# Kernel optimization log

Measured on AMD Instinct MI355X. Metric: run time of the kernel, lower is better.

## Reference

```python
import jax, jax.numpy as jnp
import numpy as np

N = 50000      # num_nodes
E = 800000     # num_edges
H = 64         # hidden_dim
L = 4          # num_layers
NH = 4         # num_heads
HD = H // NH   # head_dim


def setup_inputs() -> dict:
    key = jax.random.key(0)
    ks = iter(jax.random.split(key, 64))
    def nrm(shape, s=0.1):
        return jax.random.normal(next(ks), shape, jnp.float32) * s
    inp = dict(
        x=jax.random.normal(next(ks), (N, 4), jnp.float32),
        edge_index=jax.random.randint(next(ks), (2, E), 0, N),
        edge_attr=jax.random.normal(next(ks), (E, 2), jnp.float32),
        in_w=nrm((4, H)), in_b=jnp.zeros((H,), jnp.float32),
        conv_rw1=nrm((L, H + 2, H)), conv_rb1=jnp.zeros((L, H), jnp.float32),
        conv_rw2=nrm((L, H, H)), conv_rb2=jnp.zeros((L, H), jnp.float32),
        conv_iw1=nrm((L, H + 2, H)), conv_ib1=jnp.zeros((L, H), jnp.float32),
        conv_iw2=nrm((L, H, H)), conv_ib2=jnp.zeros((L, H), jnp.float32),
        conv_sw=nrm((L, H, 4 * H)), conv_sb=jnp.zeros((L, 4 * H), jnp.float32),
        att_qw=nrm((L, 4, H)), att_qb=jnp.zeros((L, H), jnp.float32),
        att_kw=nrm((L, 4, H)), att_kb=jnp.zeros((L, H), jnp.float32),
        att_vw=nrm((L, 4, H)), att_vb=jnp.zeros((L, H), jnp.float32),
        att_ow=nrm((L, H, 4)), att_ob=jnp.zeros((L, 4), jnp.float32),
        ln_g=jnp.ones((L, 4), jnp.float32), ln_b=jnp.zeros((L, 4), jnp.float32),
        out_w1=nrm((H, H // 2)), out_b1=jnp.zeros((H // 2,), jnp.float32),
        out_w2=nrm((H // 2, 4)), out_b2=jnp.zeros((4,), jnp.float32),
        res_w=jnp.full((L,), 0.1, jnp.float32),
    )
    return inp


def reference(x, edge_index, edge_attr, in_w, in_b,
              conv_rw1, conv_rb1, conv_rw2, conv_rb2,
              conv_iw1, conv_ib1, conv_iw2, conv_ib2,
              conv_sw, conv_sb,
              att_qw, att_qb, att_kw, att_kb, att_vw, att_vb, att_ow, att_ob,
              ln_g, ln_b, out_w1, out_b1, out_w2, out_b2, res_w):
    n = x.shape[0]
    row, col = edge_index[0], edge_index[1]
    # add_self_loops with edge_attr fill 0 (used only inside the conv)
    loops = jnp.arange(n)
    row_sl = jnp.concatenate([row, loops])
    col_sl = jnp.concatenate([col, loops])
    ea_sl = jnp.concatenate([edge_attr, jnp.zeros((n, 2), edge_attr.dtype)], axis=0)
    deg = jax.ops.segment_sum(jnp.ones((row_sl.shape[0],), x.dtype), col_sl,
                              num_segments=n)[:, None]  # >=1 due to self loops

    h = x @ in_w + in_b  # [N, H]
    for i in range(L):
        residual = x
        # ---- ComplexGraphConv (mean aggregation, source_to_target) ----
        msg_in = jnp.concatenate([h[row_sl], ea_sl], axis=-1)  # [E+N, H+2]
        real = jax.nn.relu(msg_in @ conv_rw1[i] + conv_rb1[i]) @ conv_rw2[i] + conv_rb2[i]
        imag = jax.nn.relu(msg_in @ conv_iw1[i] + conv_ib1[i]) @ conv_iw2[i] + conv_ib2[i]
        mag = jnp.sqrt(real * real + imag * imag)
        phase = jnp.arctan2(imag, real + 1e-8)
        msg = jnp.concatenate([real, imag, mag, phase], axis=-1)  # [E+N, 4H]
        agg = jax.ops.segment_sum(msg, col_sl, num_segments=n) / deg
        h4 = agg + (h @ conv_sw[i] + conv_sb[i])  # [N, 4H]
        x4 = h4[:, :4]
        # ---- ComplexGraphAttention (global edge softmax per head) ----
        Q = (x4 @ att_qw[i] + att_qb[i]).reshape(n, NH, HD)
        K = (x4 @ att_kw[i] + att_kb[i]).reshape(n, NH, HD)
        V = (x4 @ att_vw[i] + att_vb[i]).reshape(n, NH, HD)
        scores = jnp.einsum('ehd,ehd->eh', Q[row], K[col]) / np.sqrt(HD).astype(x.dtype)
        w = jax.nn.softmax(scores, axis=0)  # softmax over ALL edges (dim=0)
        att = jax.ops.segment_sum(w[:, :, None] * V[row], col,
                                  num_segments=n).reshape(n, NH * HD)
        x4 = (att @ att_ow[i] + att_ob[i]) + x4  # out_proj + residual (dropout=eval)
        # ---- LayerNorm over last dim (4) ----
        mu = x4.mean(-1, keepdims=True)
        var = x4.var(-1, keepdims=True)
        x4 = (x4 - mu) / jnp.sqrt(var + 1e-5) * ln_g[i] + ln_b[i]
        x = x4 + residual * res_w[i]
        h = x @ in_w + in_b
    pred = jnp.tanh(jax.nn.relu(h @ out_w1 + out_b1) @ out_w2 + out_b2) * 0.3
    return pred
```

## Files before the change

### kernel.cpp

```cpp
#include <hip/hip_runtime.h>
#include <hip/hip_bf16.h>
#include <hip/hip_fp16.h>

#define N_NODES 50000
#define N_EDGES 800000
#define BUCKET 64
#define EDGE_TB 3125
#define NODE_NB 3125

__device__ __forceinline__ float rdlane(float v, int k) {
    return __uint_as_float(__builtin_amdgcn_readlane(__float_as_uint(v), k));
}
template <int CTRL>
__device__ __forceinline__ float dpp_addf(float v) {
    int x = __builtin_amdgcn_update_dpp(0, __float_as_int(v), CTRL, 0xF, 0xF, true);
    return v + __int_as_float(x);
}
#define DPP_QX1  0xB1
#define DPP_QX2  0x4E
#define DPP_HM   0x141
#define DPP_RM   0x140
#define DPP_ROR4 0x124
#define DPP_ROR8 0x128
__device__ __forceinline__ float dpp_sum16(float v) {
    v = dpp_addf<DPP_QX1>(v);
    v = dpp_addf<DPP_QX2>(v);
    v = dpp_addf<DPP_HM>(v);
    v = dpp_addf<DPP_RM>(v);
    return v;
}
__device__ __forceinline__ void bsum4(float& v0, float& v1, float& v2, float& v3) {
    #pragma unroll
    for (int m = 1; m < 64; m <<= 1) {
        v0 += __shfl_xor(v0, m);
        v1 += __shfl_xor(v1, m);
        v2 += __shfl_xor(v2, m);
        v3 += __shfl_xor(v3, m);
    }
}
__device__ __forceinline__ void cvt_t4(float2 raw, float tk[4]) {
    __half2 a = ((const __half2*)&raw)[0];
    __half2 b = ((const __half2*)&raw)[1];
    float2 fa = __half22float2(a), fb = __half22float2(b);
    tk[0] = fa.x; tk[1] = fa.y; tk[2] = fb.x; tk[3] = fb.y;
}

__global__ void k_setup(const float* __restrict__ x, const float* __restrict__ in_w,
                        const float* __restrict__ in_b, const float* __restrict__ rw1,
                        const float* __restrict__ rb1, float* __restrict__ hb,
                        float4* __restrict__ xcur, unsigned* __restrict__ cntC,
                        __half* __restrict__ t,
                        const int* __restrict__ row, const int* __restrict__ col,
                        const float* __restrict__ ea, uint2* __restrict__ colEA,
                        const float* __restrict__ qw, const float* __restrict__ qb,
                        const float* __restrict__ kw, const float* __restrict__ kb,
                        const float* __restrict__ vw, const float* __restrict__ vb,
                        const float* __restrict__ ow, float* __restrict__ cst,
                        float* __restrict__ cstV) {
    int tid = threadIdx.x;
    int bid = blockIdx.x;
    if (bid < 2 * EDGE_TB) {
        if ((bid & 1) == 0) {
            int e = (bid >> 1) * 256 + tid;
            if (e < N_EDGES) {
                int c = col[e];
                unsigned slot = atomicAdd(&cntC[c], 1u);
                float2 e2 = ((const float2*)ea)[e];
                __half2 h2 = __floats2half2_rn(e2.x, e2.y);
                unsigned long long rec =
                    ((unsigned long long)(unsigned)row[e] << 32) |
                    (unsigned long long)(*reinterpret_cast<unsigned*>(&h2));
                __builtin_nontemporal_store(
                    rec, (unsigned long long*)&colEA[(size_t)c * BUCKET + slot]);
            }
            return;
        }
        int wid = ((bid >> 1) * 256 + tid) >> 6;
        int lane = tid & 63;
        int n0 = wid * 4;
        if (n0 >= N_NODES) return;
        float iw0 = in_w[lane], iw1 = in_w[64 + lane], iw2 = in_w[128 + lane], iw3 = in_w[192 + lane];
        float ibl = in_b[lane];
        float hv[4];
        #pragma unroll
        for (int i = 0; i < 4; i++) {
            int n = n0 + i;
            hv[i] = 0.f;
            if (n < N_NODES) {
                float4 xv = ((const float4*)x)[n];
                hv[i] = ibl + xv.x * iw0 + xv.y * iw1 + xv.z * iw2 + xv.w * iw3;
                hb[n * 64 + lane] = hv[i];
                if (lane == 0) xcur[n] = xv;
            }
        }
        float acc[4];
        #pragma unroll
        for (int i = 0; i < 4; i++) acc[i] = rb1[lane];
        for (int k = 0; k < 64; k++) {
            float w = rw1[k * 64 + lane];
            #pragma unroll
            for (int i = 0; i < 4; i++) acc[i] += rdlane(hv[i], k) * w;
        }
        #pragma unroll
        for (int i = 0; i < 4; i++) {
            int n = n0 + i;
            if (n < N_NODES) t[n * 64 + lane] = __float2half(acc[i]);
        }
        return;
    }
    int pb = bid - 2 * EDGE_TB;
    int m = tid;
    if (m >= 64) return;
    int d = m & 15;
    if (pb < 4) {
        int L = pb;
        const float* qwl = qw + L * 256; const float* kwl = kw + L * 256;
        const float* qbl = qb + L * 64;  const float* kbl = kb + L * 64;
        float qa[4], ka[4];
        #pragma unroll
        for (int a = 0; a < 4; a++) { qa[a] = qwl[a * 64 + m]; ka[a] = kwl[a * 64 + m]; }
        float qbm = qbl[m], kbm = kbl[m];
        float vals[25];
        int idx = 0;
        #pragma unroll
        for (int a = 0; a < 4; a++)
            #pragma unroll
            for (int b = 0; b < 4; b++) vals[idx++] = qa[a] * ka[b];
        #pragma unroll
        for (int a = 0; a < 4; a++) vals[idx++] = qa[a] * kbm;
        #pragma unroll
        for (int b = 0; b < 4; b++) vals[idx++] = qbm * ka[b];
        vals[24] = qbm * kbm;
        #pragma unroll
        for (int i = 0; i < 25; i++) {
            float v = vals[i];
            v += __shfl_xor(v, 1); v += __shfl_xor(v, 2);
            v += __shfl_xor(v, 4); v += __shfl_xor(v, 8);
            vals[i] = v;
        }
        if (d == 0) {
            float* out = cst + L * 128 + (m >> 4) * 32;
            #pragma unroll
            for (int i = 0; i < 25; i++) out[i] = vals[i] * 0.25f;
        }
    } else {
        int L = pb - 4;
        int h = m >> 4;
        const float* vwl = vw + L * 256;
        const float* vbl = vb + L * 64;
        float4 owv = ((const float4*)(ow + L * 256))[m];
        float vals[20];
        #pragma unroll
        for (int a = 0; a < 4; a++) {
            float v = vwl[a * 64 + m];
            vals[a * 4 + 0] = v * owv.x; vals[a * 4 + 1] = v * owv.y;
            vals[a * 4 + 2] = v * owv.z; vals[a * 4 + 3] = v * owv.w;
        }
        float b = vbl[m];
        vals[16] = b * owv.x; vals[17] = b * owv.y; vals[18] = b * owv.z; vals[19] = b * owv.w;
        #pragma unroll
        for (int i = 0; i < 20; i++) {
            float v = vals[i];
            v += __shfl_xor(v, 1); v += __shfl_xor(v, 2);
            v += __shfl_xor(v, 4); v += __shfl_xor(v, 8);
            vals[i] = v;
        }
        if (d == 0) {
            float* out = cstV + L * 128 + h * 32;
            #pragma unroll
            for (int i = 0; i < 20; i++) out[i] = vals[i];
        }
    }
}

__global__ void k61(const float* __restrict__ att16, const float* __restrict__ sumexpP,
                    const float4* __restrict__ x4b, const float* __restrict__ ob,
                    const float* __restrict__ g, const float* __restrict__ bb,
                    const float* __restrict__ resw, const float* __restrict__ in_w,
                    const float* __restrict__ in_b, float4* __restrict__ xcur,
                    const float* __restrict__ rw1, const float* __restrict__ rb1,
                    __half* __restrict__ t, float* __restrict__ hb) {
    int tid = threadIdx.x;
    int wid = (blockIdx.x * blockDim.x + tid) >> 6;
    int lane = tid & 63;
    int n0 = wid * 4;
    if (n0 >= N_NODES) return;
    float iw0 = in_w[lane], iw1 = in_w[64 + lane], iw2 = in_w[128 + lane], iw3 = in_w[192 + lane];
    float ibl = in_b[lane];
    float4 zp = ((const float4*)sumexpP)[lane];
    bsum4(zp.x, zp.y, zp.z, zp.w);
    int hh = (lane & 15) >> 2;
    float z = (hh == 0) ? zp.x : (hh == 1) ? zp.y : (hh == 2) ? zp.z : zp.w;
    float ob0 = ob[0], ob1 = ob[1], ob2 = ob[2], ob3 = ob[3];
    float g0 = g[0], g1 = g[1], g2 = g[2], g3 = g[3];
    float bb0 = bb[0], bb1 = bb[1], bb2 = bb[2], bb3 = bb[3];
    float rw = resw[0];
    float hv[4];
    #pragma unroll
    for (int i = 0; i < 4; i++) {
        int n = n0 + i;
        float a = 0.f;
        if (n < N_NODES && lane < 16) a = att16[n * 16 + lane] / z;
        a = dpp_addf<DPP_ROR4>(a);
        a = dpp_addf<DPP_ROR8>(a);
        float y0 = rdlane(a, 0), y1 = rdlane(a, 1), y2 = rdlane(a, 2), y3 = rdlane(a, 3);
        hv[i] = 0.f;
        if (n < N_NODES) {
            float4 x4v = x4b[n];
            y0 += ob0 + x4v.x; y1 += ob1 + x4v.y;
            y2 += ob2 + x4v.z; y3 += ob3 + x4v.w;
            float mu = 0.25f * (y0 + y1 + y2 + y3);
            float d0 = y0 - mu, d1 = y1 - mu, d2 = y2 - mu, d3 = y3 - mu;
            float var = 0.25f * (d0 * d0 + d1 * d1 + d2 * d2 + d3 * d3);
            float rs = rsqrtf(var + 1e-5f);
            float4 xold = xcur[n];
            float nn0 = d0 * rs * g0 + bb0 + xold.x * rw;
            float nn1 = d1 * rs * g1 + bb1 + xold.y * rw;
            float nn2 = d2 * rs * g2 + bb2 + xold.z * rw;
            float nn3 = d3 * rs * g3 + bb3 + xold.w * rw;
            if (lane == 0) xcur[n] = make_float4(nn0, nn1, nn2, nn3);
            hv[i] = ibl + nn0 * iw0 + nn1 * iw1 + nn2 * iw2 + nn3 * iw3;
            hb[n * 64 + lane] = hv[i];
        }
    }
    float acc[4];
    #pragma unroll
    for (int i = 0; i < 4; i++) acc[i] = rb1[lane];
    for (int k = 0; k < 64; k++) {
        float w = rw1[k * 64 + lane];
        #pragma unroll
        for (int i = 0; i < 4; i++) acc[i] += rdlane(hv[i], k) * w;
    }
    #pragma unroll
    for (int i = 0; i < 4; i++) {
        int n = n0 + i;
        if (n < N_NODES) t[n * 64 + lane] = __float2half(acc[i]);
    }
}

__global__ void k23b(const unsigned* __restrict__ cntC, const uint2* __restrict__ colEA,
                     const __half* __restrict__ t, const float* __restrict__ hb,
                     const float* __restrict__ rw1, const float* __restrict__ rw2,
                     const float* __restrict__ sw, const float* __restrict__ rb2,
                     const float* __restrict__ sb,
                     float4* __restrict__ x4b, float* __restrict__ sumexpP) {
    __shared__ float s_rw2[64][4];
    __shared__ float s_sw[64][4];
    __shared__ float s_w1[128];
    int tid = threadIdx.x;
    { int r = tid >> 2, cc = tid & 3; s_rw2[r][cc] = rw2[r * 64 + cc]; s_sw[r][cc] = sw[r * 256 + cc]; }
    if (tid < 128) s_w1[tid] = rw1[64 * 64 + tid];
    if (blockIdx.x == 0) sumexpP[tid] = 0.f;
    __syncthreads();
    int lane = tid & 63;
    int sub = lane >> 4, l16 = lane & 15;
    int gid = (blockIdx.x * blockDim.x + tid) >> 6;
    int c = gid * 4 + sub;
    if (c >= N_NODES) return;
    float w1a[4], w1b[4], wr2[4][4];
    #pragma unroll
    for (int j = 0; j < 4; j++) {
        int ch = l16 * 4 + j;
        w1a[j] = s_w1[ch];
        w1b[j] = s_w1[64 + ch];
        #pragma unroll
        for (int o = 0; o < 4; o++) wr2[j][o] = s_rw2[ch][o];
    }
    float2 trS = *(const float2*)(t + (size_t)c * 64 + l16 * 4);
    float4 hv = ((const float4*)hb)[c * 16 + l16];
    float a0 = 0.f, a1 = 0.f, a2 = 0.f, a3 = 0.f;
    float b0 = 0.f, b1 = 0.f, b2 = 0.f, b3 = 0.f;
    {
        float tk[4];
        cvt_t4(trS, tk);
        #pragma unroll
        for (int j = 0; j < 4; j++) {
            int ch = l16 * 4 + j;
            float rr = fmaxf(tk[j], 0.f);
            a0 += rr * wr2[j][0]; a1 += rr * wr2[j][1];
            a2 += rr * wr2[j][2]; a3 += rr * wr2[j][3];
            float hk = (j == 0) ? hv.x : (j == 1) ? hv.y : (j == 2) ? hv.z : hv.w;
            b0 += hk * s_sw[ch][0]; b1 += hk * s_sw[ch][1];
            b2 += hk * s_sw[ch][2]; b3 += hk * s_sw[ch][3];
        }
    }
    int cnt = (int)cntC[c];
    const uint2* rowE = colEA + (size_t)c * BUCKET;
    const uint2 zr = make_uint2(0u, 0u);
    const float2 z2 = make_float2(0.f, 0.f);
    int p = 0;
    bool vld0 = p < cnt;
    uint2 erA = vld0 ? rowE[0] : zr;
    float2 trA = vld0 ? *(const float2*)(t + (size_t)erA.y * 64 + l16 * 4) : z2;
    int pn = 1;
    bool vld1 = pn < cnt;
    uint2 erB = vld1 ? rowE[1] : zr;
    while (vld0) {
        float2 trB = vld1 ? *(const float2*)(t + (size_t)erB.y * 64 + l16 * 4) : z2;
        int pnn = pn + 1;
        bool vld2 = pnn < cnt;
        uint2 erC = vld2 ? rowE[pnn] : zr;
        float tk[4];
        cvt_t4(trA, tk);
        __half2 eh = *reinterpret_cast<const __half2*>(&erA.x);
        float2 ef = __half22float2(eh);
        float ex = ef.x, ey = ef.y;
        #pragma unroll
        for (int j = 0; j < 4; j++) {
            float pre = tk[j] + ex * w1a[j] + ey * w1b[j];
            float rr = fmaxf(pre, 0.f);
            a0 += rr * wr2[j][0]; a1 += rr * wr2[j][1];
            a2 += rr * wr2[j][2]; a3 += rr * wr2[j][3];
        }
        erA = erB; trA = trB; erB = erC;
        vld0 = vld1; vld1 = vld2; pn = pnn;
    }
    a0 = dpp_sum16(a0); a1 = dpp_sum16(a1); a2 = dpp_sum16(a2); a3 = dpp_sum16(a3);
    b0 = dpp_sum16(b0); b1 = dpp_sum16(b1); b2 = dpp_sum16(b2); b3 = dpp_sum16(b3);
    if (l16 == 0) {
        float idg = 1.f / (float)(cnt + 1);
        x4b[c] = make_float4(a0 * idg + b0 + rb2[0] + sb[0],
                             a1 * idg + b1 + rb2[1] + sb[1],
                             a2 * idg + b2 + rb2[2] + sb[2],
                             a3 * idg + b3 + rb2[3] + sb[3]);
    }
}

__global__ void k5_att(const unsigned* __restrict__ cntC, const uint2* __restrict__ colEA,
                       const float4* __restrict__ x4b, const float* __restrict__ cst,
                       const float* __restrict__ cstV, float* __restrict__ att16,
                       float* __restrict__ sumexpP) {
    __shared__ float zs[8][4];
    int tid = threadIdx.x;
    int lane = tid & 63;
    int wv = tid >> 6;
    int hw = lane >> 5;
    int l32 = lane & 31;
    int sub = l32 >> 4;
    int d = l32 & 15, h = d >> 2, a = d & 3;
    int c = ((blockIdx.x * blockDim.x + tid) >> 6) * 2 + hw;
    float zval = 0.f;
    if (c < N_NODES) {
        const float* C = cst + h * 32;
        float4 xc = x4b[c];
        float g0 = xc.x * C[0]  + xc.y * C[1]  + xc.z * C[2]  + xc.w * C[3]  + C[16];
        float g1 = xc.x * C[4]  + xc.y * C[5]  + xc.z * C[6]  + xc.w * C[7]  + C[17];
        float g2 = xc.x * C[8]  + xc.y * C[9]  + xc.z * C[10] + xc.w * C[11] + C[18];
        float g3 = xc.x * C[12] + xc.y * C[13] + xc.z * C[14] + xc.w * C[15] + C[19];
        float base = C[20] * xc.x + C[21] * xc.y + C[22] * xc.z + C[23] * xc.w + C[24];
        int cnt = (int)cntC[c];
        const unsigned* rowY = (const unsigned*)(colEA + (size_t)c * BUCKET);
        const float4 z4 = make_float4(0.f, 0.f, 0.f, 0.f);
        float S = 0.f, z = 0.f;
        int p = sub;
        bool vld0 = p < cnt;
        float4 xr = z4;
        if (vld0) xr = x4b[rowY[2 * p + 1]];
        int pn = p + 2;
        bool vld1 = pn < cnt;
        unsigned rn = vld1 ? rowY[2 * pn + 1] : 0u;
        while (vld0) {
            float4 xrn = z4;
            if (vld1) xrn = x4b[rn];
            int pnn = pn + 2;
            bool vld2 = pnn < cnt;
            unsigned rnn = vld2 ? rowY[2 * pnn + 1] : 0u;
            float s = xr.x * g0 + xr.y * g1 + xr.z * g2 + xr.w * g3 + base;
            float ex = __expf(s);
            float xa = (a == 0) ? xr.x : (a == 1) ? xr.y : (a == 2) ? xr.z : xr.w;
            S += ex * xa;
            z += ex;
            xr = xrn; rn = rnn; vld0 = vld1; vld1 = vld2; pn = pnn;
        }
        S += __shfl_xor(S, 16);
        z += __shfl_xor(z, 16);
        const float* V = cstV + h * 32;
        float c0 = S * V[a * 4 + 0], c1 = S * V[a * 4 + 1];
        float c2 = S * V[a * 4 + 2], c3 = S * V[a * 4 + 3];
        c0 = dpp_addf<DPP_QX1>(c0); c1 = dpp_addf<DPP_QX1>(c1);
        c2 = dpp_addf<DPP_QX1>(c2); c3 = dpp_addf<DPP_QX1>(c3);
        c0 = dpp_addf<DPP_QX2>(c0); c1 = dpp_addf<DPP_QX2>(c1);
        c2 = dpp_addf<DPP_QX2>(c2); c3 = dpp_addf<DPP_QX2>(c3);
        float my = (a == 0) ? c0 : (a == 1) ? c1 : (a == 2) ? c2 : c3;
        if (sub == 0) att16[c * 16 + d] = my + z * V[16 + a];
        zval = z;
    }
    if (sub == 0 && a == 0) zs[wv * 2 + hw][h] = zval;
    __syncthreads();
    if (tid < 4) {
        float acc = 0.f;
        #pragma unroll
        for (int q = 0; q < 8; q++) acc += zs[q][tid];
        atomicAdd(&sumexpP[((blockIdx.x & 63) << 2) + tid], acc);
    }
}

__global__ void k6pred(const float* __restrict__ att16, const float* __restrict__ sumexpP,
                       const float4* __restrict__ x4b, const float* __restrict__ ob,
                       const float* __restrict__ g, const float* __restrict__ bb,
                       const float* __restrict__ resw, const float4* __restrict__ xcur,
                       const float* __restrict__ in_w, const float* __restrict__ in_b,
                       const float* __restrict__ w1, const float* __restrict__ b1,
                       const float* __restrict__ w2, const float* __restrict__ b2,
                       float* __restrict__ out) {
    int tid = threadIdx.x;
    int node = (blockIdx.x * blockDim.x + tid) >> 6;
    int lane = tid & 63;
    if (node >= N_NODES) return;
    float4 zp = ((const float4*)sumexpP)[lane];
    bsum4(zp.x, zp.y, zp.z, zp.w);
    int hh = (lane & 15) >> 2;
    float z = (hh == 0) ? zp.x : (hh == 1) ? zp.y : (hh == 2) ? zp.z : zp.w;
    float a = 0.f;
    if (lane < 16) a = att16[node * 16 + lane] / z;
    a = dpp_addf<DPP_ROR4>(a);
    a = dpp_addf<DPP_ROR8>(a);
    float y0 = rdlane(a, 0), y1 = rdlane(a, 1), y2 = rdlane(a, 2), y3 = rdlane(a, 3);
    float4 x4v = x4b[node];
    y0 += ob[0] + x4v.x; y1 += ob[1] + x4v.y;
    y2 += ob[2] + x4v.z; y3 += ob[3] + x4v.w;
    float mu = 0.25f * (y0 + y1 + y2 + y3);
    float d0 = y0 - mu, d1 = y1 - mu, d2 = y2 - mu, d3 = y3 - mu;
    float var = 0.25f * (d0 * d0 + d1 * d1 + d2 * d2 + d3 * d3);
    float rs = rsqrtf(var + 1e-5f);
    float4 xold = xcur[node];
    float rw = resw[0];
    float n0 = d0 * rs * g[0] + bb[0] + xold.x * rw;
    float n1 = d1 * rs * g[1] + bb[1] + xold.y * rw;
    float n2 = d2 * rs * g[2] + bb[2] + xold.z * rw;
    float n3 = d3 * rs * g[3] + bb[3] + xold.w * rw;
    float hv = in_b[lane] + n0 * in_w[lane] + n1 * in_w[64 + lane]
             + n2 * in_w[128 + lane] + n3 * in_w[192 + lane];
    int j2 = lane & 31;
    float m = b1[j2];
    for (int k = 0; k < 64; k++) m += rdlane(hv, k) * w1[k * 32 + j2];
    m = fmaxf(m, 0.f);
    float4 w2v = ((const float4*)w2)[j2];
    float v0 = m * w2v.x, v1 = m * w2v.y, v2 = m * w2v.z, v3 = m * w2v.w;
    bsum4(v0, v1, v2, v3);
    float o0 = tanhf(0.5f * v0 + b2[0]) * 0.3f;
    float o1 = tanhf(0.5f * v1 + b2[1]) * 0.3f;
    float o2 = tanhf(0.5f * v2 + b2[2]) * 0.3f;
    float o3 = tanhf(0.5f * v3 + b2[3]) * 0.3f;
    if (lane == 0) ((float4*)out)[node] = make_float4(o0, o1, o2, o3);
}

extern "C" void kernel_launch(void* const* d_in, const int* in_sizes, int n_in,
                              void* d_out, int out_size, void* d_ws, size_t ws_size,
                              hipStream_t stream) {
    const float* x        = (const float*)d_in[0];
    const int*   ei       = (const int*)d_in[1];
    const float* ea       = (const float*)d_in[2];
    const float* in_w     = (const float*)d_in[3];
    const float* in_b     = (const float*)d_in[4];
    const float* conv_rw1 = (const float*)d_in[5];
    const float* conv_rb1 = (const float*)d_in[6];
    const float* conv_rw2 = (const float*)d_in[7];
    const float* conv_rb2 = (const float*)d_in[8];
    const float* conv_sw  = (const float*)d_in[13];
    const float* conv_sb  = (const float*)d_in[14];
    const float* att_qw   = (const float*)d_in[15];
    const float* att_qb   = (const float*)d_in[16];
    const float* att_kw   = (const float*)d_in[17];
    const float* att_kb   = (const float*)d_in[18];
    const float* att_vw   = (const float*)d_in[19];
    const float* att_vb   = (const float*)d_in[20];
    const float* att_ow   = (const float*)d_in[21];
    const float* att_ob   = (const float*)d_in[22];
    const float* ln_g     = (const float*)d_in[23];
    const float* ln_b     = (const float*)d_in[24];
    const float* out_w1   = (const float*)d_in[25];
    const float* out_b1   = (const float*)d_in[26];
    const float* out_w2   = (const float*)d_in[27];
    const float* out_b2   = (const float*)d_in[28];
    const float* res_w    = (const float*)d_in[29];

    const int* row = ei;
    const int* col = ei + N_EDGES;

    char* ws = (char*)d_ws;
    size_t off = 0;
    auto alloc = [&](size_t bytes) -> void* {
        void* p = ws + off;
        off = (off + bytes + 255) & ~(size_t)255;
        return p;
    };
    unsigned* cntC     = (unsigned*)alloc(N_NODES * 4);
    uint2*    colEA    = (uint2*)alloc((size_t)N_NODES * BUCKET * 8);
    __half*   tbuf     = (__half*)alloc((size_t)N_NODES * 64 * 2);
    float*    hb       = (float*)alloc((size_t)N_NODES * 64 * 4);
    float*    att16    = (float*)alloc((size_t)N_NODES * 16 * 4);
    float4*   x4b      = (float4*)alloc((size_t)N_NODES * 16);
    float4*   xcur     = (float4*)alloc((size_t)N_NODES * 16);
    float*    cst      = (float*)alloc(4 * 128 * 4);
    float*    cstV     = (float*)alloc(4 * 128 * 4);
    float*    sumexpP  = (float*)alloc(64 * 4 * 4);

    dim3 b256(256);
    int nodeBlocks2 = (N_NODES + 7) / 8;
    int nodeBlocks4 = (N_NODES + 15) / 16;
    int dstBlocks   = (N_NODES + 15) / 16;

    hipMemsetAsync(cntC, 0, N_NODES * 4, stream);
    k_setup<<<2 * EDGE_TB + 8, b256, 0, stream>>>(
        x, in_w, in_b, conv_rw1, conv_rb1, hb, xcur, cntC, tbuf,
        row, col, ea, colEA,
        att_qw, att_qb, att_kw, att_kb, att_vw, att_vb, att_ow, cst, cstV);

    for (int i = 0; i < 4; i++) {
        const float* rw1 = conv_rw1 + i * 66 * 64;
        const float* rb1 = conv_rb1 + i * 64;
        const float* rw2 = conv_rw2 + i * 64 * 64;
        const float* rb2 = conv_rb2 + i * 64;
        const float* swl = conv_sw + i * 64 * 256;
        const float* sbl = conv_sb + i * 256;

        if (i > 0) {
            k61<<<nodeBlocks4, b256, 0, stream>>>(att16, sumexpP, x4b,
                                                  att_ob + (i - 1) * 4, ln_g + (i - 1) * 4,
                                                  ln_b + (i - 1) * 4, res_w + (i - 1),
                                                  in_w, in_b, xcur,
                                                  rw1, rb1, tbuf, hb);
        }
        k23b<<<dstBlocks, b256, 0, stream>>>(cntC, colEA, tbuf, hb,
                                             rw1, rw2, swl, rb2, sbl, x4b, sumexpP);
        k5_att<<<nodeBlocks2, b256, 0, stream>>>(cntC, colEA, x4b, cst + i * 128,
                                                 cstV + i * 128, att16, sumexpP);
    }
    k6pred<<<(N_NODES + 3) / 4, b256, 0, stream>>>(att16, sumexpP, x4b, att_ob + 12, ln_g + 12,
                                            ln_b + 12, res_w + 3, xcur, in_w, in_b,
                                            out_w1, out_b1, out_w2, out_b2, (float*)d_out);
}
```

Measured before the change: 497.2 us.

## Fold input projection into conv weights and gather 4-wide node state per edge

Since h = x @ in_w + in_b is an affine map of the 4-wide node state, the first conv layer's pre-activation and the skip projection are folded into small precomputed matrices (in_w·rw1, in_b·rw1+rb1, in_w·sw). The per-node 64-wide fp16 t buffer and fp32 h buffer are no longer materialized. The edge loop now gathers a 16-byte float4 of xcur per source node instead of a 64-channel fp16 slice, and recomputes the 64-channel preactivation with extra FMAs per edge. This trades DRAM/L2 gather traffic and the k61 matmul for more ALU work per edge, and it also removes fp16 rounding of t.

```diff
diff --git a/kernel.cpp b/kernel.cpp
--- a/kernel.cpp
+++ b/kernel.cpp
@@ -6,7 +6,7 @@
 #define N_EDGES 800000
 #define BUCKET 64
 #define EDGE_TB 3125
-#define NODE_NB 3125
+#define COPY_NB 196
 
 __device__ __forceinline__ float rdlane(float v, int k) {
     return __uint_as_float(__builtin_amdgcn_readlane(__float_as_uint(v), k));
@@ -38,77 +38,43 @@
         v3 += __shfl_xor(v3, m);
     }
 }
-__device__ __forceinline__ void cvt_t4(float2 raw, float tk[4]) {
-    __half2 a = ((const __half2*)&raw)[0];
-    __half2 b = ((const __half2*)&raw)[1];
-    float2 fa = __half22float2(a), fb = __half22float2(b);
-    tk[0] = fa.x; tk[1] = fa.y; tk[2] = fb.x; tk[3] = fb.y;
-}
-
-__global__ void k_setup(const float* __restrict__ x, const float* __restrict__ in_w,
-                        const float* __restrict__ in_b, const float* __restrict__ rw1,
-                        const float* __restrict__ rb1, float* __restrict__ hb,
-                        float4* __restrict__ xcur, unsigned* __restrict__ cntC,
-                        __half* __restrict__ t,
+
+__global__ void k_setup(const float* __restrict__ x, unsigned* __restrict__ cntC,
+                        float4* __restrict__ xcur,
                         const int* __restrict__ row, const int* __restrict__ col,
                         const float* __restrict__ ea, uint2* __restrict__ colEA,
                         const float* __restrict__ qw, const float* __restrict__ qb,
                         const float* __restrict__ kw, const float* __restrict__ kb,
                         const float* __restrict__ vw, const float* __restrict__ vb,
-                        const float* __restrict__ ow, float* __restrict__ cst,
-                        float* __restrict__ cstV) {
+                        const float* __restrict__ ow,
+                        const float* __restrict__ in_w, const float* __restrict__ in_b,
+                        const float* __restrict__ rw1all, const float* __restrict__ rb1all,
+                        const float* __restrict__ swall,
+                        float* __restrict__ cst, float* __restrict__ cstV,
+                        float* __restrict__ cstM) {
     int tid = threadIdx.x;
     int bid = blockIdx.x;
-    if (bid < 2 * EDGE_TB) {
-        if ((bid & 1) == 0) {
-            int e = (bid >> 1) * 256 + tid;
-            if (e < N_EDGES) {
-                int c = col[e];
-                unsigned slot = atomicAdd(&cntC[c], 1u);
-                float2 e2 = ((const float2*)ea)[e];
-                __half2 h2 = __floats2half2_rn(e2.x, e2.y);
-                unsigned long long rec =
-                    ((unsigned long long)(unsigned)row[e] << 32) |
-                    (unsigned long long)(*reinterpret_cast<unsigned*>(&h2));
-                __builtin_nontemporal_store(
-                    rec, (unsigned long long*)&colEA[(size_t)c * BUCKET + slot]);
-            }
-            return;
-        }
-        int wid = ((bid >> 1) * 256 + tid) >> 6;
-        int lane = tid & 63;
-        int n0 = wid * 4;
-        if (n0 >= N_NODES) return;
-        float iw0 = in_w[lane], iw1 = in_w[64 + lane], iw2 = in_w[128 + lane], iw3 = in_w[192 + lane];
-        float ibl = in_b[lane];
-        float hv[4];
-        #pragma unroll
-        for (int i = 0; i < 4; i++) {
-            int n = n0 + i;
-            hv[i] = 0.f;
-            if (n < N_NODES) {
-                float4 xv = ((const float4*)x)[n];
-                hv[i] = ibl + xv.x * iw0 + xv.y * iw1 + xv.z * iw2 + xv.w * iw3;
-                hb[n * 64 + lane] = hv[i];
-                if (lane == 0) xcur[n] = xv;
-            }
-        }
-        float acc[4];
-        #pragma unroll
-        for (int i = 0; i < 4; i++) acc[i] = rb1[lane];
-        for (int k = 0; k < 64; k++) {
-            float w = rw1[k * 64 + lane];
-            #pragma unroll
-            for (int i = 0; i < 4; i++) acc[i] += rdlane(hv[i], k) * w;
-        }
-        #pragma unroll
-        for (int i = 0; i < 4; i++) {
-            int n = n0 + i;
-            if (n < N_NODES) t[n * 64 + lane] = __float2half(acc[i]);
+    if (bid < EDGE_TB) {
+        int e = bid * 256 + tid;
+        if (e < N_EDGES) {
+            int c = col[e];
+            unsigned slot = atomicAdd(&cntC[c], 1u);
+            float2 e2 = ((const float2*)ea)[e];
+            __half2 h2 = __floats2half2_rn(e2.x, e2.y);
+            unsigned long long rec =
+                ((unsigned long long)(unsigned)row[e] << 32) |
+                (unsigned long long)(*reinterpret_cast<unsigned*>(&h2));
+            __builtin_nontemporal_store(
+                rec, (unsigned long long*)&colEA[(size_t)c * BUCKET + slot]);
         }
         return;
     }
-    int pb = bid - 2 * EDGE_TB;
+    if (bid < EDGE_TB + COPY_NB) {
+        int n = (bid - EDGE_TB) * 256 + tid;
+        if (n < N_NODES) xcur[n] = ((const float4*)x)[n];
+        return;
+    }
+    int pb = bid - (EDGE_TB + COPY_NB);
     int m = tid;
     if (m >= 64) return;
     int d = m & 15;
@@ -143,7 +109,7 @@
             #pragma unroll
             for (int i = 0; i < 25; i++) out[i] = vals[i] * 0.25f;
         }
-    } else {
+    } else if (pb < 8) {
         int L = pb - 4;
         int h = m >> 4;
         const float* vwl = vw + L * 256;
@@ -170,23 +136,47 @@
             #pragma unroll
             for (int i = 0; i < 20; i++) out[i] = vals[i];
         }
+    } else {
+        int L = pb - 8;
+        const float* rw1 = rw1all + L * 66 * 64;
+        const float* rb1 = rb1all + L * 64;
+        const float* sw  = swall + L * 64 * 256;
+        float* M = cstM + L * 384;
+        float bacc = rb1[m];
+        float w0 = 0.f, w1 = 0.f, w2 = 0.f, w3 = 0.f;
+        for (int k = 0; k < 64; k++) {
+            float r = rw1[k * 64 + m];
+            bacc += in_b[k] * r;
+            w0 += in_w[k] * r;
+            w1 += in_w[64 + k] * r;
+            w2 += in_w[128 + k] * r;
+            w3 += in_w[192 + k] * r;
+        }
+        M[m * 4 + 0] = w0; M[m * 4 + 1] = w1; M[m * 4 + 2] = w2; M[m * 4 + 3] = w3;
+        M[256 + m] = bacc;
+        if (m < 16) {
+            int a = m >> 2, o = m & 3;
+            float sacc = 0.f;
+            for (int k = 0; k < 64; k++) sacc += in_w[a * 64 + k] * sw[k * 256 + o];
+            M[320 + m] = sacc;
+        }
+        if (m < 4) {
+            float sacc = 0.f;
+            for (int k = 0; k < 64; k++) sacc += in_b[k] * sw[k * 256 + m];
+            M[336 + m] = sacc;
+        }
     }
 }
 
 __global__ void k61(const float* __restrict__ att16, const float* __restrict__ sumexpP,
                     const float4* __restrict__ x4b, const float* __restrict__ ob,
                     const float* __restrict__ g, const float* __restrict__ bb,
-                    const float* __restrict__ resw, const float* __restrict__ in_w,
-                    const float* __restrict__ in_b, float4* __restrict__ xcur,
-                    const float* __restrict__ rw1, const float* __restrict__ rb1,
-                    __half* __restrict__ t, float* __restrict__ hb) {
+                    const float* __restrict__ resw, float4* __restrict__ xcur) {
     int tid = threadIdx.x;
     int wid = (blockIdx.x * blockDim.x + tid) >> 6;
     int lane = tid & 63;
     int n0 = wid * 4;
     if (n0 >= N_NODES) return;
-    float iw0 = in_w[lane], iw1 = in_w[64 + lane], iw2 = in_w[128 + lane], iw3 = in_w[192 + lane];
-    float ibl = in_b[lane];
     float4 zp = ((const float4*)sumexpP)[lane];
     bsum4(zp.x, zp.y, zp.z, zp.w);
     int hh = (lane & 15) >> 2;
@@ -195,7 +185,6 @@
     float g0 = g[0], g1 = g[1], g2 = g[2], g3 = g[3];
     float bb0 = bb[0], bb1 = bb[1], bb2 = bb[2], bb3 = bb[3];
     float rw = resw[0];
-    float hv[4];
     #pragma unroll
     for (int i = 0; i < 4; i++) {
         int n = n0 + i;
@@ -204,7 +193,6 @@
         a = dpp_addf<DPP_ROR4>(a);
         a = dpp_addf<DPP_ROR8>(a);
         float y0 = rdlane(a, 0), y1 = rdlane(a, 1), y2 = rdlane(a, 2), y3 = rdlane(a, 3);
-        hv[i] = 0.f;
         if (n < N_NODES) {
             float4 x4v = x4b[n];
             y0 += ob0 + x4v.x; y1 += ob1 + x4v.y;
@@ -219,37 +207,27 @@
             float nn2 = d2 * rs * g2 + bb2 + xold.z * rw;
             float nn3 = d3 * rs * g3 + bb3 + xold.w * rw;
             if (lane == 0) xcur[n] = make_float4(nn0, nn1, nn2, nn3);
-            hv[i] = ibl + nn0 * iw0 + nn1 * iw1 + nn2 * iw2 + nn3 * iw3;
-            hb[n * 64 + lane] = hv[i];
-        }
-    }
-    float acc[4];
-    #pragma unroll
-    for (int i = 0; i < 4; i++) acc[i] = rb1[lane];
-    for (int k = 0; k < 64; k++) {
-        float w = rw1[k * 64 + lane];
-        #pragma unroll
-        for (int i = 0; i < 4; i++) acc[i] += rdlane(hv[i], k) * w;
-    }
-    #pragma unroll
-    for (int i = 0; i < 4; i++) {
-        int n = n0 + i;
-        if (n < N_NODES) t[n * 64 + lane] = __float2half(acc[i]);
+        }
     }
 }
 
 __global__ void k23b(const unsigned* __restrict__ cntC, const uint2* __restrict__ colEA,
-                     const __half* __restrict__ t, const float* __restrict__ hb,
-                     const float* __restrict__ rw1, const float* __restrict__ rw2,
-                     const float* __restrict__ sw, const float* __restrict__ rb2,
-                     const float* __restrict__ sb,
+                     const float4* __restrict__ xcur, const float* __restrict__ rw1,
+                     const float* __restrict__ rw2, const float* __restrict__ cstM,
+                     const float* __restrict__ rb2, const float* __restrict__ sb,
                      float4* __restrict__ x4b, float* __restrict__ sumexpP) {
     __shared__ float s_rw2[64][4];
-    __shared__ float s_sw[64][4];
+    __shared__ float s_weff[64][4];
     __shared__ float s_w1[128];
+    __shared__ float s_beff[64];
+    __shared__ float s_sw16[16];
+    __shared__ float s_sbe[4];
     int tid = threadIdx.x;
-    { int r = tid >> 2, cc = tid & 3; s_rw2[r][cc] = rw2[r * 64 + cc]; s_sw[r][cc] = sw[r * 256 + cc]; }
+    { int r = tid >> 2, cc = tid & 3; s_rw2[r][cc] = rw2[r * 64 + cc]; s_weff[r][cc] = cstM[tid]; }
     if (tid < 128) s_w1[tid] = rw1[64 * 64 + tid];
+    if (tid < 64) s_beff[tid] = cstM[256 + tid];
+    if (tid < 16) s_sw16[tid] = cstM[320 + tid];
+    if (tid < 4)  s_sbe[tid]  = cstM[336 + tid];
     if (blockIdx.x == 0) sumexpP[tid] = 0.f;
     __syncthreads();
     int lane = tid & 63;
@@ -257,68 +235,65 @@
     int gid = (blockIdx.x * blockDim.x + tid) >> 6;
     int c = gid * 4 + sub;
     if (c >= N_NODES) return;
-    float w1a[4], w1b[4], wr2[4][4];
+    float wf[4][4], bfr[4], w1a[4], w1b[4], wr2r[4][4];
     #pragma unroll
     for (int j = 0; j < 4; j++) {
         int ch = l16 * 4 + j;
+        #pragma unroll
+        for (int a = 0; a < 4; a++) wf[j][a] = s_weff[ch][a];
+        bfr[j] = s_beff[ch];
         w1a[j] = s_w1[ch];
         w1b[j] = s_w1[64 + ch];
         #pragma unroll
-        for (int o = 0; o < 4; o++) wr2[j][o] = s_rw2[ch][o];
-    }
-    float2 trS = *(const float2*)(t + (size_t)c * 64 + l16 * 4);
-    float4 hv = ((const float4*)hb)[c * 16 + l16];
+        for (int o = 0; o < 4; o++) wr2r[j][o] = s_rw2[ch][o];
+    }
+    float4 xc = xcur[c];
     float a0 = 0.f, a1 = 0.f, a2 = 0.f, a3 = 0.f;
-    float b0 = 0.f, b1 = 0.f, b2 = 0.f, b3 = 0.f;
-    {
-        float tk[4];
-        cvt_t4(trS, tk);
-        #pragma unroll
-        for (int j = 0; j < 4; j++) {
-            int ch = l16 * 4 + j;
-            float rr = fmaxf(tk[j], 0.f);
-            a0 += rr * wr2[j][0]; a1 += rr * wr2[j][1];
-            a2 += rr * wr2[j][2]; a3 += rr * wr2[j][3];
-            float hk = (j == 0) ? hv.x : (j == 1) ? hv.y : (j == 2) ? hv.z : hv.w;
-            b0 += hk * s_sw[ch][0]; b1 += hk * s_sw[ch][1];
-            b2 += hk * s_sw[ch][2]; b3 += hk * s_sw[ch][3];
-        }
+    #pragma unroll
+    for (int j = 0; j < 4; j++) {
+        float tk = bfr[j] + xc.x * wf[j][0] + xc.y * wf[j][1]
+                 + xc.z * wf[j][2] + xc.w * wf[j][3];
+        float rr = fmaxf(tk, 0.f);
+        a0 += rr * wr2r[j][0]; a1 += rr * wr2r[j][1];
+        a2 += rr * wr2r[j][2]; a3 += rr * wr2r[j][3];
     }
     int cnt = (int)cntC[c];
     const uint2* rowE = colEA + (size_t)c * BUCKET;
     const uint2 zr = make_uint2(0u, 0u);
-    const float2 z2 = make_float2(0.f, 0.f);
+    const float4 z4 = make_float4(0.f, 0.f, 0.f, 0.f);
     int p = 0;
     bool vld0 = p < cnt;
     uint2 erA = vld0 ? rowE[0] : zr;
-    float2 trA = vld0 ? *(const float2*)(t + (size_t)erA.y * 64 + l16 * 4) : z2;
+    float4 xrA = vld0 ? xcur[erA.y] : z4;
     int pn = 1;
     bool vld1 = pn < cnt;
     uint2 erB = vld1 ? rowE[1] : zr;
     while (vld0) {
-        float2 trB = vld1 ? *(const float2*)(t + (size_t)erB.y * 64 + l16 * 4) : z2;
+        float4 xrB = vld1 ? xcur[erB.y] : z4;
         int pnn = pn + 1;
         bool vld2 = pnn < cnt;
         uint2 erC = vld2 ? rowE[pnn] : zr;
-        float tk[4];
-        cvt_t4(trA, tk);
         __half2 eh = *reinterpret_cast<const __half2*>(&erA.x);
         float2 ef = __half22float2(eh);
-        float ex = ef.x, ey = ef.y;
         #pragma unroll
         for (int j = 0; j < 4; j++) {
-            float pre = tk[j] + ex * w1a[j] + ey * w1b[j];
+            float tk = bfr[j] + xrA.x * wf[j][0] + xrA.y * wf[j][1]
+                     + xrA.z * wf[j][2] + xrA.w * wf[j][3];
+            float pre = tk + ef.x * w1a[j] + ef.y * w1b[j];
             float rr = fmaxf(pre, 0.f);
-            a0 += rr * wr2[j][0]; a1 += rr * wr2[j][1];
-            a2 += rr * wr2[j][2]; a3 += rr * wr2[j][3];
-        }
-        erA = erB; trA = trB; erB = erC;
+            a0 += rr * wr2r[j][0]; a1 += rr * wr2r[j][1];
+            a2 += rr * wr2r[j][2]; a3 += rr * wr2r[j][3];
+        }
+        erA = erB; xrA = xrB; erB = erC;
         vld0 = vld1; vld1 = vld2; pn = pnn;
     }
     a0 = dpp_sum16(a0); a1 = dpp_sum16(a1); a2 = dpp_sum16(a2); a3 = dpp_sum16(a3);
-    b0 = dpp_sum16(b0); b1 = dpp_sum16(b1); b2 = dpp_sum16(b2); b3 = dpp_sum16(b3);
     if (l16 == 0) {
         float idg = 1.f / (float)(cnt + 1);
+        float b0 = xc.x * s_sw16[0] + xc.y * s_sw16[4] + xc.z * s_sw16[8]  + xc.w * s_sw16[12] + s_sbe[0];
+        float b1 = xc.x * s_sw16[1] + xc.y * s_sw16[5] + xc.z * s_sw16[9]  + xc.w * s_sw16[13] + s_sbe[1];
+        float b2 = xc.x * s_sw16[2] + xc.y * s_sw16[6] + xc.z * s_sw16[10] + xc.w * s_sw16[14] + s_sbe[2];
+        float b3 = xc.x * s_sw16[3] + xc.y * s_sw16[7] + xc.z * s_sw16[11] + xc.w * s_sw16[15] + s_sbe[3];
         x4b[c] = make_float4(a0 * idg + b0 + rb2[0] + sb[0],
                              a1 * idg + b1 + rb2[1] + sb[1],
                              a2 * idg + b2 + rb2[2] + sb[2],
@@ -487,13 +462,12 @@
     };
     unsigned* cntC     = (unsigned*)alloc(N_NODES * 4);
     uint2*    colEA    = (uint2*)alloc((size_t)N_NODES * BUCKET * 8);
-    __half*   tbuf     = (__half*)alloc((size_t)N_NODES * 64 * 2);
-    float*    hb       = (float*)alloc((size_t)N_NODES * 64 * 4);
     float*    att16    = (float*)alloc((size_t)N_NODES * 16 * 4);
     float4*   x4b      = (float4*)alloc((size_t)N_NODES * 16);
     float4*   xcur     = (float4*)alloc((size_t)N_NODES * 16);
     float*    cst      = (float*)alloc(4 * 128 * 4);
     float*    cstV     = (float*)alloc(4 * 128 * 4);
+    float*    cstM     = (float*)alloc(4 * 384 * 4);
     float*    sumexpP  = (float*)alloc(64 * 4 * 4);
 
     dim3 b256(256);
@@ -502,28 +476,26 @@
     int dstBlocks   = (N_NODES + 15) / 16;
 
     hipMemsetAsync(cntC, 0, N_NODES * 4, stream);
-    k_setup<<<2 * EDGE_TB + 8, b256, 0, stream>>>(
-        x, in_w, in_b, conv_rw1, conv_rb1, hb, xcur, cntC, tbuf,
-        row, col, ea, colEA,
-        att_qw, att_qb, att_kw, att_kb, att_vw, att_vb, att_ow, cst, cstV);
+    k_setup<<<EDGE_TB + COPY_NB + 12, b256, 0, stream>>>(
+        x, cntC, xcur, row, col, ea, colEA,
+        att_qw, att_qb, att_kw, att_kb, att_vw, att_vb, att_ow,
+        in_w, in_b, conv_rw1, conv_rb1, conv_sw,
+        cst, cstV, cstM);
 
     for (int i = 0; i < 4; i++) {
         const float* rw1 = conv_rw1 + i * 66 * 64;
-        const float* rb1 = conv_rb1 + i * 64;
         const float* rw2 = conv_rw2 + i * 64 * 64;
         const float* rb2 = conv_rb2 + i * 64;
-        const float* swl = conv_sw + i * 64 * 256;
         const float* sbl = conv_sb + i * 256;
 
         if (i > 0) {
             k61<<<nodeBlocks4, b256, 0, stream>>>(att16, sumexpP, x4b,
                                                   att_ob + (i - 1) * 4, ln_g + (i - 1) * 4,
                                                   ln_b + (i - 1) * 4, res_w + (i - 1),
-                                                  in_w, in_b, xcur,
-                                                  rw1, rb1, tbuf, hb);
-        }
-        k23b<<<dstBlocks, b256, 0, stream>>>(cntC, colEA, tbuf, hb,
-                                             rw1, rw2, swl, rb2, sbl, x4b, sumexpP);
+                                                  xcur);
+        }
+        k23b<<<dstBlocks, b256, 0, stream>>>(cntC, colEA, xcur, rw1, rw2,
+                                             cstM + i * 384, rb2, sbl, x4b, sumexpP);
         k5_att<<<nodeBlocks2, b256, 0, stream>>>(cntC, colEA, x4b, cst + i * 128,
                                                  cstV + i * 128, att16, sumexpP);
     }
```

After: 487.8 us. About the same (-1.9%).
